# Performance work log

Measured on AMD Instinct MI355X. Metric: run time of the kernel, lower is better.

The kernel has to match this reference:

```python
import jax, jax.numpy as jnp
import numpy as np

NEG_SLOPE = 0.2  # PyG GATConv default negative_slope
EPS = 1e-16


def gat_conv(x, src, dst, num_nodes, W, a_src, a_dst, bias, heads, out_c, concat):
    """PyG-style GATConv (eval mode, self-loops already appended).
    x: [N, F_in]; src/dst: [E] (edge j->i with src=j, dst=i).
    W: [F_in, heads*out_c]; a_src/a_dst: [heads, out_c]; bias: [heads*out_c] or [out_c].
    """
    xw = (x @ W).reshape(num_nodes, heads, out_c)          # [N, H, C]
    alpha_src = jnp.sum(xw * a_src, axis=-1)               # [N, H]
    alpha_dst = jnp.sum(xw * a_dst, axis=-1)               # [N, H]
    e = jax.nn.leaky_relu(alpha_src[src] + alpha_dst[dst], NEG_SLOPE)  # [E, H]
    # numerically stable segment softmax over edges grouped by destination node
    m = jax.ops.segment_max(e, dst, num_segments=num_nodes)            # [N, H]
    e = jnp.exp(e - m[dst])
    denom = jax.ops.segment_sum(e, dst, num_segments=num_nodes)        # [N, H]
    alpha = e / (denom[dst] + EPS)                                     # [E, H]
    # weighted scatter-sum aggregation of source messages
    out = jax.ops.segment_sum(xw[src] * alpha[:, :, None], dst, num_segments=num_nodes)  # [N, H, C]
    if concat:
        out = out.reshape(num_nodes, heads * out_c)
    else:
        out = out.mean(axis=1)
    return out + bias


def setup_inputs() -> dict:
    key = jax.random.key(0)
    ks = jax.random.split(key, 12)
    N, E = 50000, 800000
    F_in, Hid, H1, Out = 512, 32, 8, 64

    def xavier(k, shape, gain=1.414):
        fan_in, fan_out = shape[0], shape[-1] if len(shape) == 2 else int(np.prod(shape[1:]))
        a = gain * np.sqrt(6.0 / (fan_in + fan_out))
        return jax.random.uniform(k, shape, jnp.float32, -a, a)

    x = jax.random.normal(ks[0], (N, F_in), jnp.float32)
    edge_index = jax.random.randint(ks[1], (2, E), 0, N, jnp.int64)

    W1 = xavier(ks[2], (F_in, H1 * Hid))
    a_src1 = xavier(ks[3], (H1, Hid))
    a_dst1 = xavier(ks[4], (H1, Hid))
    b1 = jnp.zeros((H1 * Hid,), jnp.float32)

    W2 = xavier(ks[5], (H1 * Hid, Out))
    a_src2 = xavier(ks[6], (1, Out))
    a_dst2 = xavier(ks[7], (1, Out))
    b2 = jnp.zeros((Out,), jnp.float32)

    return {"x": x, "edge_index": edge_index,
            "W1": W1, "a_src1": a_src1, "a_dst1": a_dst1, "b1": b1,
            "W2": W2, "a_src2": a_src2, "a_dst2": a_dst2, "b2": b2}


def reference(x, edge_index, W1, a_src1, a_dst1, b1, W2, a_src2, a_dst2, b2):
    N = x.shape[0]
    # add self-loops (PyG GATConv default add_self_loops=True)
    loop = jnp.arange(N, dtype=edge_index.dtype)
    src = jnp.concatenate([edge_index[0], loop])
    dst = jnp.concatenate([edge_index[1], loop])

    # eval mode: all dropouts are identity
    h = gat_conv(x, src, dst, N, W1, a_src1, a_dst1, b1, heads=8, out_c=32, concat=True)
    h = jax.nn.elu(h)
    h = gat_conv(h, src, dst, N, W2, a_src2, a_dst2, b2, heads=1, out_c=64, concat=False)
    return jax.nn.log_softmax(h, axis=1)
```

## Files before the change

kernel.cpp:

```cpp
#include <hip/hip_runtime.h>
#include <hip/hip_bf16.h>


typedef __attribute__((ext_vector_type(8)))  __bf16          bf16x8;
typedef __attribute__((ext_vector_type(8)))  unsigned short  ushort8;
typedef __attribute__((ext_vector_type(16))) float           f32x16;

#define NEG_SLOPE 0.2f
#define EPS_GAT 1e-16f

static __device__ __forceinline__ float lrelu(float x) {
    return x > 0.0f ? x : NEG_SLOPE * x;
}
static __device__ __forceinline__ unsigned short f2bf(float f) {
    unsigned u = __float_as_uint(f);
    return (unsigned short)((u + 0x7fffu + ((u >> 16) & 1u)) >> 16);
}
static __device__ __forceinline__ float bf2f(unsigned short v) {
    return __uint_as_float(((unsigned)v) << 16);
}
static __device__ __forceinline__ unsigned encf(float x) {
    unsigned u = __float_as_uint(x);
    return (u >> 31) ? ~u : (u | 0x80000000u);
}
static __device__ __forceinline__ float decf(unsigned e) {
    unsigned u = (e >> 31) ? (e & 0x7fffffffu) : ~e;
    return __uint_as_float(u);
}

__global__ void k_hist_w(const void* __restrict__ eix, int* __restrict__ counts,
                         int E, int EB,
                         const float* __restrict__ W1, const float* __restrict__ W2,
                         unsigned short* __restrict__ w1t, unsigned short* __restrict__ w2t) {
    int b = blockIdx.x;
    if (b < EB) {
        int i = b * 256 + threadIdx.x;
        unsigned w = ((const unsigned*)eix)[2 * min(i, E - 1) + 1];
        bool is64 = (__syncthreads_or((int)(w != 0u)) == 0);
        if (i < E) {
            int d = is64 ? (int)((const long long*)eix)[E + i]
                         : ((const int*)eix)[E + i];
            atomicAdd(&counts[d], 1);
        }
    } else {
        int t = (b - EB) * 256 + threadIdx.x;
        if (t < 512 * 256) {
            int k = t >> 8, m = t & 255;
            w1t[m * 512 + k] = f2bf(W1[t]);
        } else {
            int u = t - 512 * 256;
            if (u < 256 * 64) {
                int k = u >> 6, m = u & 63;
                w2t[m * 256 + k] = f2bf(W2[u]);
            }
        }
    }
}

__global__ void k_scan1(const int* __restrict__ counts, int* __restrict__ rowp,
                        int* __restrict__ bsum, int N) {
    __shared__ int s[256];
    int t = threadIdx.x, i = blockIdx.x * 256 + t;
    int v = (i < N) ? counts[i] : 0;
    s[t] = v;
    __syncthreads();
    for (int off = 1; off < 256; off <<= 1) {
        int u = (t >= off) ? s[t - off] : 0;
        __syncthreads();
        s[t] += u;
        __syncthreads();
    }
    if (i < N) rowp[i] = s[t] - v;
    if (t == 255) bsum[blockIdx.x] = s[255];
}

__global__ void k_scan2(const int* __restrict__ bsum, int* __restrict__ boff,
                        int* __restrict__ rowp_last, int NB) {
    __shared__ int s[256];
    int t = threadIdx.x;
    int v = (t < NB) ? bsum[t] : 0;
    s[t] = v;
    __syncthreads();
    for (int off = 1; off < 256; off <<= 1) {
        int u = (t >= off) ? s[t - off] : 0;
        __syncthreads();
        s[t] += u;
        __syncthreads();
    }
    if (t < NB) boff[t] = s[t] - v;
    if (t == 255) *rowp_last = s[255];
}

__global__ void k_scan3(int* __restrict__ rowp, int* __restrict__ cursor,
                        const int* __restrict__ boff, int N) {
    int i = blockIdx.x * 256 + threadIdx.x;
    if (i < N) {
        int r = rowp[i] + boff[blockIdx.x];
        rowp[i] = r;
        cursor[i] = r;
    }
}

__global__ void k_fill(const void* __restrict__ eix, int* __restrict__ cursor,
                       int* __restrict__ ssrc, int E) {
    int i = blockIdx.x * 256 + threadIdx.x;
    unsigned w = ((const unsigned*)eix)[2 * min(i, E - 1) + 1];
    bool is64 = (__syncthreads_or((int)(w != 0u)) == 0);
    if (i >= E) return;
    int s, d;
    if (is64) {
        s = (int)((const long long*)eix)[i];
        d = (int)((const long long*)eix)[E + i];
    } else {
        s = ((const int*)eix)[i];
        d = ((const int*)eix)[E + i];
    }
    int pos = atomicAdd(&cursor[d], 1);
    ssrc[pos] = s;
}

template <int BM, int BN, int NT, bool AF32, bool OUTBF>
__global__ __launch_bounds__(NT) void k_gemm(const void* __restrict__ Ain,
                                             const unsigned short* __restrict__ Bt,
                                             void* __restrict__ Cout, int Nrows, int K) {
    constexpr int LD = 40;
    __shared__ __align__(16) unsigned short As[BM * LD];
    __shared__ __align__(16) unsigned short Bs[BN * LD];
    const int tid = threadIdx.x;
    const int blockRow = blockIdx.x * BM;
    const int wave = tid >> 6, lane = tid & 63;
    constexpr int WR = BM / 64;
    const int wr = wave % WR, wc = wave / WR;
    const int m = lane & 31;
    const int ksel = (lane >> 5) * 8;

    f32x16 acc00{}, acc01{}, acc10{}, acc11{};

    for (int kt = 0; kt < K; kt += 32) {
        if constexpr (AF32) {
            const float* A = (const float*)Ain;
            for (int idx = tid; idx < BM * 4; idx += NT) {
                int r = idx >> 2, kc = (idx & 3) * 8;
                int grow = blockRow + r;
                union { ushort8 u; __hip_bfloat162 h[4]; } cv;
                if (grow < Nrows) {
                    const float* ap = A + (size_t)grow * K + kt + kc;
                    float4 x0 = *(const float4*)ap;
                    float4 x1 = *(const float4*)(ap + 4);
                    cv.h[0] = __float22bfloat162_rn(make_float2(x0.x, x0.y));
                    cv.h[1] = __float22bfloat162_rn(make_float2(x0.z, x0.w));
                    cv.h[2] = __float22bfloat162_rn(make_float2(x1.x, x1.y));
                    cv.h[3] = __float22bfloat162_rn(make_float2(x1.z, x1.w));
                } else {
                    cv.u = ushort8{};
                }
                *(ushort8*)&As[r * LD + kc] = cv.u;
            }
        } else {
            const unsigned short* A = (const unsigned short*)Ain;
            for (int idx = tid; idx < BM * 4; idx += NT) {
                int r = idx >> 2, kc = (idx & 3) * 8;
                int grow = blockRow + r;
                ushort8 o{};
                if (grow < Nrows) o = *(const ushort8*)(A + (size_t)grow * K + kt + kc);
                *(ushort8*)&As[r * LD + kc] = o;
            }
        }
        for (int idx = tid; idx < BN * 4; idx += NT) {
            int r = idx >> 2, kc = (idx & 3) * 8;
            *(ushort8*)&Bs[r * LD + kc] = *(const ushort8*)(Bt + (size_t)r * K + kt + kc);
        }
        __syncthreads();

        #pragma unroll
        for (int kk = 0; kk < 32; kk += 16) {
            bf16x8 a0 = *(const bf16x8*)&As[(wr * 64 +      m) * LD + kk + ksel];
            bf16x8 a1 = *(const bf16x8*)&As[(wr * 64 + 32 + m) * LD + kk + ksel];
            bf16x8 b0 = *(const bf16x8*)&Bs[(wc * 64 +      m) * LD + kk + ksel];
            bf16x8 b1 = *(const bf16x8*)&Bs[(wc * 64 + 32 + m) * LD + kk + ksel];
            acc00 = __builtin_amdgcn_mfma_f32_32x32x16_bf16(a0, b0, acc00, 0, 0, 0);
            acc01 = __builtin_amdgcn_mfma_f32_32x32x16_bf16(a0, b1, acc01, 0, 0, 0);
            acc10 = __builtin_amdgcn_mfma_f32_32x32x16_bf16(a1, b0, acc10, 0, 0, 0);
            acc11 = __builtin_amdgcn_mfma_f32_32x32x16_bf16(a1, b1, acc11, 0, 0, 0);
        }
        __syncthreads();
    }

    const int dcol = wc * 64 + (lane & 31);
    const int dquad = 4 * (lane >> 5);
    auto store_tile = [&](const f32x16& a, int rt, int ct) {
        #pragma unroll
        for (int r = 0; r < 16; ++r) {
            int row = blockRow + wr * 64 + rt * 32 + (r & 3) + 8 * (r >> 2) + dquad;
            if (row < Nrows) {
                size_t off = (size_t)row * BN + dcol + ct * 32;
                if constexpr (OUTBF) ((unsigned short*)Cout)[off] = f2bf(a[r]);
                else                 ((float*)Cout)[off] = a[r];
            }
        }
    };
    store_tile(acc00, 0, 0); store_tile(acc01, 0, 1);
    store_tile(acc10, 1, 0); store_tile(acc11, 1, 1);
}

__global__ void k_alpha(const unsigned short* __restrict__ xw, const float* __restrict__ a_s,
                        const float* __restrict__ a_d, float* __restrict__ os,
                        float* __restrict__ od, unsigned* __restrict__ Menc,
                        int NH, int H, int C) {
    __shared__ float red[256];
    int t = blockIdx.x * 256 + threadIdx.x;
    float s = -1e30f, d = 0.f;
    if (t < NH) {
        int n = t / H, h = t - n * H;
        const unsigned short* row = xw + (size_t)n * H * C + h * C;
        s = 0.f;
        for (int c = 0; c < C; c += 8) {
            ushort8 v = *(const ushort8*)(row + c);
            #pragma unroll
            for (int q = 0; q < 8; ++q) {
                float f = bf2f(v[q]);
                s += f * a_s[h * C + c + q];
                d += f * a_d[h * C + c + q];
            }
        }
        os[t] = s; od[t] = d;
    }
    red[threadIdx.x] = s;
    __syncthreads();
    for (int off = 128; off >= H; off >>= 1) {
        if (threadIdx.x < off) red[threadIdx.x] = fmaxf(red[threadIdx.x], red[threadIdx.x + off]);
        __syncthreads();
    }
    if ((int)threadIdx.x < H) atomicMax(&Menc[threadIdx.x], encf(red[threadIdx.x]));
}

__global__ __launch_bounds__(256) void k_agg_l1(
        const unsigned short* __restrict__ xw1, const float* __restrict__ asrc,
        const float* __restrict__ adst, const unsigned* __restrict__ Menc,
        const float* __restrict__ b1, const int* __restrict__ rp,
        const int* __restrict__ ssrc, unsigned short* __restrict__ hbf, int N) {
    int wid = (blockIdx.x * 256 + threadIdx.x) >> 6;
    if (wid >= N) return;
    int lane = threadIdx.x & 63;
    int g  = lane >> 4;
    int q  = lane & 15;
    int f0 = q * 16;
    int h  = q >> 1;
    int ih = wid * 8 + h;
    float ad = adst[ih];
    float m  = lrelu(decf(Menc[h]) + ad);
    float acc[16];
    float s;
    {
        float w = (g == 0) ? __expf(lrelu(asrc[ih] + ad) - m) : 0.0f;
        const unsigned short* pr = xw1 + (size_t)wid * 256 + f0;
        ushort8 lo = *(const ushort8*)pr;
        ushort8 hi = *(const ushort8*)(pr + 8);
        s = w;
        #pragma unroll
        for (int i = 0; i < 8; ++i) { acc[i] = w * bf2f(lo[i]); acc[8 + i] = w * bf2f(hi[i]); }
    }
    int e0 = rp[wid], e1 = rp[wid + 1];
    if (e0 < e1) {
        int eA = e0;
        bool vA = eA + g < e1;
        int jA = ssrc[min(eA + g, e1 - 1)];
        float asA = asrc[jA * 8 + h];
        const unsigned short* pA = xw1 + (size_t)jA * 256 + f0;
        ushort8 loA = *(const ushort8*)pA;
        ushort8 hiA = *(const ushort8*)(pA + 8);
        int eB = e0 + 4;
        bool hasB = eB < e1;
        bool vB = false; int jB = 0;
        if (hasB) { vB = eB + g < e1; jB = ssrc[min(eB + g, e1 - 1)]; }
        int eC = e0 + 8;
        while (true) {
            bool hasC = eC < e1;
            bool vC = false; int jC = 0;
            if (hasC) { vC = eC + g < e1; jC = ssrc[min(eC + g, e1 - 1)]; }
            float asB = 0.f; ushort8 loB{}, hiB{};
            if (hasB) {
                asB = asrc[jB * 8 + h];
                const unsigned short* pB = xw1 + (size_t)jB * 256 + f0;
                loB = *(const ushort8*)pB;
                hiB = *(const ushort8*)(pB + 8);
            }
            float w = vA ? __expf(lrelu(asA + ad) - m) : 0.0f;
            s += w;
            #pragma unroll
            for (int i = 0; i < 8; ++i) {
                acc[i]     += w * bf2f(loA[i]);
                acc[8 + i] += w * bf2f(hiA[i]);
            }
            if (!hasB) break;
            vA = vB; asA = asB; loA = loB; hiA = hiB;
            jB = jC; vB = vC; hasB = hasC;
            eC += 4;
        }
    }
    s += __shfl_xor(s, 16, 64);
    s += __shfl_xor(s, 32, 64);
    #pragma unroll
    for (int i = 0; i < 16; ++i) {
        acc[i] += __shfl_xor(acc[i], 16, 64);
        acc[i] += __shfl_xor(acc[i], 32, 64);
    }
    float inv = 1.0f / (s + EPS_GAT);
    int fw = f0 + g * 4;
    ushort4 o;
    #pragma unroll
    for (int i = 0; i < 4; ++i) {
        float v = acc[g * 4 + i] * inv + b1[fw + i];
        v = v > 0.f ? v : expm1f(v);
        ((unsigned short*)&o)[i] = f2bf(v);
    }
    *(ushort4*)(hbf + (size_t)wid * 256 + fw) = o;
}

__global__ __launch_bounds__(256) void k_agg_l2(
        const unsigned short* __restrict__ xw2, const float* __restrict__ asrc,
        const float* __restrict__ adst, const unsigned* __restrict__ Menc,
        const float* __restrict__ b2, const int* __restrict__ rp,
        const int* __restrict__ ssrc, float* __restrict__ out, int N) {
    int wid = (blockIdx.x * 256 + threadIdx.x) >> 6;
    if (wid >= N) return;
    int lane = threadIdx.x & 63;
    int g  = lane >> 3;
    int q  = lane & 7;
    int f0 = q * 8;
    float ad = adst[wid];
    float m = lrelu(decf(Menc[0]) + ad);
    float acc[8];
    float s;
    {
        float w = (g == 0) ? __expf(lrelu(asrc[wid] + ad) - m) : 0.0f;
        ushort8 xv = *(const ushort8*)(xw2 + (size_t)wid * 64 + f0);
        s = w;
        #pragma unroll
        for (int i = 0; i < 8; ++i) acc[i] = w * bf2f(xv[i]);
    }
    int e0 = rp[wid], e1 = rp[wid + 1];
    if (e0 < e1) {
        int eA = e0;
        bool vA = eA + g < e1;
        int jA = ssrc[min(eA + g, e1 - 1)];
        float asA = asrc[jA];
        ushort8 xvA = *(const ushort8*)(xw2 + (size_t)jA * 64 + f0);
        int eB = e0 + 8;
        bool hasB = eB < e1;
        bool vB = false; int jB = 0;
        if (hasB) { vB = eB + g < e1; jB = ssrc[min(eB + g, e1 - 1)]; }
        int eC = e0 + 16;
        while (true) {
            bool hasC = eC < e1;
            bool vC = false; int jC = 0;
            if (hasC) { vC = eC + g < e1; jC = ssrc[min(eC + g, e1 - 1)]; }
            float asB = 0.f; ushort8 xvB{};
            if (hasB) {
                asB = asrc[jB];
                xvB = *(const ushort8*)(xw2 + (size_t)jB * 64 + f0);
            }
            float w = vA ? __expf(lrelu(asA + ad) - m) : 0.0f;
            s += w;
            #pragma unroll
            for (int i = 0; i < 8; ++i) acc[i] += w * bf2f(xvA[i]);
            if (!hasB) break;
            vA = vB; asA = asB; xvA = xvB;
            jB = jC; vB = vC; hasB = hasC;
            eC += 8;
        }
    }
    s += __shfl_xor(s, 8, 64);
    s += __shfl_xor(s, 16, 64);
    s += __shfl_xor(s, 32, 64);
    #pragma unroll
    for (int i = 0; i < 8; ++i) {
        acc[i] += __shfl_xor(acc[i], 8, 64);
        acc[i] += __shfl_xor(acc[i], 16, 64);
        acc[i] += __shfl_xor(acc[i], 32, 64);
    }
    float inv = 1.0f / (s + EPS_GAT);
    float val[8];
    float mx = -1e30f;
    #pragma unroll
    for (int i = 0; i < 8; ++i) {
        val[i] = acc[i] * inv + b2[f0 + i];
        mx = fmaxf(mx, val[i]);
    }
    #pragma unroll
    for (int off = 4; off > 0; off >>= 1) mx = fmaxf(mx, __shfl_xor(mx, off, 64));
    float sm = 0.f;
    #pragma unroll
    for (int i = 0; i < 8; ++i) sm += __expf(val[i] - mx);
    #pragma unroll
    for (int off = 4; off > 0; off >>= 1) sm += __shfl_xor(sm, off, 64);
    float lse = mx + logf(sm);
    if (g == 0) {
        float4 o0 = make_float4(val[0] - lse, val[1] - lse, val[2] - lse, val[3] - lse);
        float4 o1 = make_float4(val[4] - lse, val[5] - lse, val[6] - lse, val[7] - lse);
        *(float4*)(out + (size_t)wid * 64 + f0)     = o0;
        *(float4*)(out + (size_t)wid * 64 + f0 + 4) = o1;
    }
}

static inline int cdiv(int a, int b) { return (a + b - 1) / b; }

extern "C" void kernel_launch(void* const* d_in, const int* in_sizes, int n_in,
                              void* d_out, int out_size, void* d_ws, size_t ws_size,
                              hipStream_t stream) {
    const float* x   = (const float*)d_in[0];
    const void*  eix = d_in[1];
    const float* W1  = (const float*)d_in[2];
    const float* as1 = (const float*)d_in[3];
    const float* ad1 = (const float*)d_in[4];
    const float* b1  = (const float*)d_in[5];
    const float* W2  = (const float*)d_in[6];
    const float* as2 = (const float*)d_in[7];
    const float* ad2 = (const float*)d_in[8];
    const float* b2  = (const float*)d_in[9];
    float* out = (float*)d_out;

    const int N = in_sizes[0] / 512;
    const int E = in_sizes[1] / 2;
    const int EB = cdiv(E, 256);
    const int WB = cdiv(512 * 256 + 256 * 64, 256);
    const int NB = cdiv(N, 256);
    const int NB1 = cdiv(N * 8, 256);
    const int NB2 = cdiv(N, 256);
    (void)n_in; (void)out_size; (void)ws_size;

    char* base = (char*)d_ws;
    size_t o = 0;
    auto alloc = [&](size_t bytes) -> char* {
        o = (o + 255) & ~(size_t)255;
        char* p = base + o;
        o += bytes;
        return p;
    };
    unsigned short* xw1b  = (unsigned short*)alloc((size_t)N * 256 * 2);
    unsigned short* hbf   = (unsigned short*)alloc((size_t)N * 256 * 2);
    unsigned short* xw2b  = (unsigned short*)alloc((size_t)N * 64 * 2);
    float*          asrc1 = (float*)alloc((size_t)N * 8 * 4);
    float*          adst1 = (float*)alloc((size_t)N * 8 * 4);
    float*          asrc2 = (float*)alloc((size_t)N * 4);
    float*          adst2 = (float*)alloc((size_t)N * 4);
    size_t zero_begin = (o + 255) & ~(size_t)255;
    unsigned*       Menc  = (unsigned*)alloc(16 * 4);
    int*            counts= (int*)alloc((size_t)N * 4);
    size_t zero_end = o;
    int*            cursor= (int*)alloc((size_t)N * 4);
    int*            rowp  = (int*)alloc((size_t)(N + 1) * 4);
    int*            bsum  = (int*)alloc(256 * 4);
    int*            boff  = (int*)alloc(256 * 4);
    unsigned short* w1t   = (unsigned short*)alloc(512 * 256 * 2);
    unsigned short* w2t   = (unsigned short*)alloc(256 * 64 * 2);
    int*            ssrc  = (int*)alloc((size_t)E * 4);

    hipMemsetAsync(base + zero_begin, 0, zero_end - zero_begin, stream);

    k_hist_w<<<EB + WB, 256, 0, stream>>>(eix, counts, E, EB, W1, W2, w1t, w2t);
    k_scan1<<<NB, 256, 0, stream>>>(counts, rowp, bsum, N);
    k_scan2<<<1, 256, 0, stream>>>(bsum, boff, rowp + N, NB);
    k_scan3<<<NB, 256, 0, stream>>>(rowp, cursor, boff, N);
    k_fill<<<EB, 256, 0, stream>>>(eix, cursor, ssrc, E);

    k_gemm<128, 256, 512, true, true><<<cdiv(N, 128), 512, 0, stream>>>(x, w1t, xw1b, N, 512);
    k_alpha<<<NB1, 256, 0, stream>>>(xw1b, as1, ad1, asrc1, adst1, Menc, N * 8, 8, 32);
    k_agg_l1<<<cdiv(N * 64, 256), 256, 0, stream>>>(xw1b, asrc1, adst1, Menc, b1,
                                                    rowp, ssrc, hbf, N);
    k_gemm<256, 64, 256, false, true><<<cdiv(N, 256), 256, 0, stream>>>(hbf, w2t, xw2b, N, 256);
    k_alpha<<<NB2, 256, 0, stream>>>(xw2b, as2, ad2, asrc2, adst2, Menc + 8, N, 1, 64);
    k_agg_l2<<<cdiv(N * 64, 256), 256, 0, stream>>>(xw2b, asrc2, adst2, Menc + 8, b2,
                                                    rowp, ssrc, out, N);
}
```

Before: 425.8 us.

## Deepen gather pipeline, use packed FMA, add occupancy hints, retile GEMMs

Both aggregation kernels move to a deeper software pipeline: neighbor indices are fetched two groups ahead and feature rows one group ahead, so gather latency is hidden. The bf16 unpack and accumulate now use packed v_pk_fma_f32 through inline asm, and launch_bounds request 6 waves per SIMD. Separately, both GEMM launches switch to smaller row tiles and fewer threads per block, giving more blocks. The aim is lower gather latency and ALU cost in aggregation and better load balance in the GEMMs, at the cost of more register pressure and smaller GEMM tiles that may reuse weights less.

Result: slower. 456.2 us (+7.1%).

```diff
diff --git a/kernel.cpp b/kernel.cpp
--- a/kernel.cpp
+++ b/kernel.cpp
@@ -5,6 +5,7 @@
 typedef __attribute__((ext_vector_type(8)))  __bf16          bf16x8;
 typedef __attribute__((ext_vector_type(8)))  unsigned short  ushort8;
 typedef __attribute__((ext_vector_type(16))) float           f32x16;
+typedef __attribute__((ext_vector_type(2)))  float           f32x2;
 
 #define NEG_SLOPE 0.2f
 #define EPS_GAT 1e-16f
@@ -234,22 +235,22 @@
     if ((int)threadIdx.x < H) atomicMax(&Menc[threadIdx.x], encf(red[threadIdx.x]));
 }
 
-__global__ __launch_bounds__(256) void k_agg_l1(
+__global__ __launch_bounds__(256, 6) void k_agg_l1(
         const unsigned short* __restrict__ xw1, const float* __restrict__ asrc,
         const float* __restrict__ adst, const unsigned* __restrict__ Menc,
         const float* __restrict__ b1, const int* __restrict__ rp,
         const int* __restrict__ ssrc, unsigned short* __restrict__ hbf, int N) {
     int wid = (blockIdx.x * 256 + threadIdx.x) >> 6;
     if (wid >= N) return;
-    int lane = threadIdx.x & 63;
-    int g  = lane >> 4;
-    int q  = lane & 15;
-    int f0 = q * 16;
-    int h  = q >> 1;
-    int ih = wid * 8 + h;
-    float ad = adst[ih];
-    float m  = lrelu(decf(Menc[h]) + ad);
-    float acc[16];
+    const int lane = threadIdx.x & 63;
+    const int g  = lane >> 4;
+    const int q  = lane & 15;
+    const int f0 = q * 16;
+    const int h  = q >> 1;
+    const int ih = wid * 8 + h;
+    const float ad = adst[ih];
+    const float m  = lrelu(decf(Menc[h]) + ad);
+    f32x2 acc[8];
     float s;
     {
         float w = (g == 0) ? __expf(lrelu(asrc[ih] + ad) - m) : 0.0f;
@@ -257,134 +258,198 @@
         ushort8 lo = *(const ushort8*)pr;
         ushort8 hi = *(const ushort8*)(pr + 8);
         s = w;
+        const unsigned* dl = (const unsigned*)&lo;
+        const unsigned* dh = (const unsigned*)&hi;
         #pragma unroll
-        for (int i = 0; i < 8; ++i) { acc[i] = w * bf2f(lo[i]); acc[8 + i] = w * bf2f(hi[i]); }
-    }
-    int e0 = rp[wid], e1 = rp[wid + 1];
+        for (int p = 0; p < 4; ++p) {
+            acc[p].x     = w * __uint_as_float(dl[p] << 16);
+            acc[p].y     = w * __uint_as_float(dl[p] & 0xffff0000u);
+            acc[4 + p].x = w * __uint_as_float(dh[p] << 16);
+            acc[4 + p].y = w * __uint_as_float(dh[p] & 0xffff0000u);
+        }
+    }
+    const int e0 = rp[wid], e1 = rp[wid + 1];
     if (e0 < e1) {
-        int eA = e0;
-        bool vA = eA + g < e1;
-        int jA = ssrc[min(eA + g, e1 - 1)];
-        float asA = asrc[jA * 8 + h];
-        const unsigned short* pA = xw1 + (size_t)jA * 256 + f0;
-        ushort8 loA = *(const ushort8*)pA;
-        ushort8 hiA = *(const ushort8*)(pA + 8);
-        int eB = e0 + 4;
-        bool hasB = eB < e1;
-        bool vB = false; int jB = 0;
-        if (hasB) { vB = eB + g < e1; jB = ssrc[min(eB + g, e1 - 1)]; }
-        int eC = e0 + 8;
-        while (true) {
-            bool hasC = eC < e1;
-            bool vC = false; int jC = 0;
-            if (hasC) { vC = eC + g < e1; jC = ssrc[min(eC + g, e1 - 1)]; }
-            float asB = 0.f; ushort8 loB{}, hiB{};
-            if (hasB) {
-                asB = asrc[jB * 8 + h];
-                const unsigned short* pB = xw1 + (size_t)jB * 256 + f0;
-                loB = *(const ushort8*)pB;
-                hiB = *(const ushort8*)(pB + 8);
-            }
-            float w = vA ? __expf(lrelu(asA + ad) - m) : 0.0f;
+        const int NQ = (e1 - e0 + 3) >> 2;
+
+        auto LDJ = [&](int base, int& j, bool& v) {
+            v = base + g < e1;
+            j = ssrc[min(base + g, e1 - 1)];
+        };
+        auto LDD = [&](int j, float& as, ushort8& lo, ushort8& hi) {
+            as = asrc[j * 8 + h];
+            const unsigned short* p = xw1 + ((size_t)j << 8) + f0;
+            lo = *(const ushort8*)p;
+            hi = *(const ushort8*)(p + 8);
+        };
+        auto CONS = [&](bool v, float as, const ushort8& lo, const ushort8& hi) {
+            float w = v ? __expf(lrelu(as + ad) - m) : 0.0f;
             s += w;
+            f32x2 wp; wp.x = w; wp.y = w;
+            const unsigned* dl = (const unsigned*)&lo;
+            const unsigned* dh = (const unsigned*)&hi;
             #pragma unroll
-            for (int i = 0; i < 8; ++i) {
-                acc[i]     += w * bf2f(loA[i]);
-                acc[8 + i] += w * bf2f(hiA[i]);
-            }
-            if (!hasB) break;
-            vA = vB; asA = asB; loA = loB; hiA = hiB;
-            jB = jC; vB = vC; hasB = hasC;
-            eC += 4;
-        }
+            for (int p = 0; p < 4; ++p) {
+                f32x2 x;
+                x.x = __uint_as_float(dl[p] << 16);
+                x.y = __uint_as_float(dl[p] & 0xffff0000u);
+                asm("v_pk_fma_f32 %0, %1, %2, %3"
+                    : "=v"(acc[p]) : "v"(x), "v"(wp), "v"(acc[p]));
+            }
+            #pragma unroll
+            for (int p = 0; p < 4; ++p) {
+                f32x2 x;
+                x.x = __uint_as_float(dh[p] << 16);
+                x.y = __uint_as_float(dh[p] & 0xffff0000u);
+                asm("v_pk_fma_f32 %0, %1, %2, %3"
+                    : "=v"(acc[4 + p]) : "v"(x), "v"(wp), "v"(acc[4 + p]));
+            }
+        };
+
+        int j0, j1, j2, j3; bool v0, v1, v2, v3;
+        float as0, as1; ushort8 lo0, hi0, lo1, hi1;
+        LDJ(e0,      j0, v0);
+        LDJ(e0 + 4,  j1, v1);
+        LDD(j0, as0, lo0, hi0);
+        LDJ(e0 + 8,  j2, v2);
+        LDD(j1, as1, lo1, hi1);
+        LDJ(e0 + 12, j3, v3);
+
+        #pragma unroll 2
+        for (int k = 0; k < NQ - 2; ++k) {
+            int jN; bool vN;
+            LDJ(e0 + 4 * k + 16, jN, vN);
+            float as2; ushort8 lo2, hi2;
+            LDD(j2, as2, lo2, hi2);
+            CONS(v0, as0, lo0, hi0);
+            v0 = v1; as0 = as1; lo0 = lo1; hi0 = hi1;
+            v1 = v2; as1 = as2; lo1 = lo2; hi1 = hi2;
+            v2 = v3; j2 = j3;
+            v3 = vN; j3 = jN;
+        }
+        CONS(v0, as0, lo0, hi0);
+        if (NQ >= 2) CONS(v1, as1, lo1, hi1);
     }
     s += __shfl_xor(s, 16, 64);
     s += __shfl_xor(s, 32, 64);
     #pragma unroll
-    for (int i = 0; i < 16; ++i) {
-        acc[i] += __shfl_xor(acc[i], 16, 64);
-        acc[i] += __shfl_xor(acc[i], 32, 64);
+    for (int p = 0; p < 8; ++p) {
+        acc[p].x += __shfl_xor(acc[p].x, 16, 64);
+        acc[p].x += __shfl_xor(acc[p].x, 32, 64);
+        acc[p].y += __shfl_xor(acc[p].y, 16, 64);
+        acc[p].y += __shfl_xor(acc[p].y, 32, 64);
     }
     float inv = 1.0f / (s + EPS_GAT);
+    f32x2 p0 = (g & 2) ? ((g & 1) ? acc[6] : acc[4]) : ((g & 1) ? acc[2] : acc[0]);
+    f32x2 p1 = (g & 2) ? ((g & 1) ? acc[7] : acc[5]) : ((g & 1) ? acc[3] : acc[1]);
     int fw = f0 + g * 4;
+    float vv[4] = { p0.x, p0.y, p1.x, p1.y };
     ushort4 o;
     #pragma unroll
     for (int i = 0; i < 4; ++i) {
-        float v = acc[g * 4 + i] * inv + b1[fw + i];
+        float v = vv[i] * inv + b1[fw + i];
         v = v > 0.f ? v : expm1f(v);
         ((unsigned short*)&o)[i] = f2bf(v);
     }
     *(ushort4*)(hbf + (size_t)wid * 256 + fw) = o;
 }
 
-__global__ __launch_bounds__(256) void k_agg_l2(
+__global__ __launch_bounds__(256, 6) void k_agg_l2(
         const unsigned short* __restrict__ xw2, const float* __restrict__ asrc,
         const float* __restrict__ adst, const unsigned* __restrict__ Menc,
         const float* __restrict__ b2, const int* __restrict__ rp,
         const int* __restrict__ ssrc, float* __restrict__ out, int N) {
     int wid = (blockIdx.x * 256 + threadIdx.x) >> 6;
     if (wid >= N) return;
-    int lane = threadIdx.x & 63;
-    int g  = lane >> 3;
-    int q  = lane & 7;
-    int f0 = q * 8;
-    float ad = adst[wid];
-    float m = lrelu(decf(Menc[0]) + ad);
-    float acc[8];
+    const int lane = threadIdx.x & 63;
+    const int g  = lane >> 3;
+    const int q  = lane & 7;
+    const int f0 = q * 8;
+    const float ad = adst[wid];
+    const float m = lrelu(decf(Menc[0]) + ad);
+    f32x2 acc[4];
     float s;
     {
         float w = (g == 0) ? __expf(lrelu(asrc[wid] + ad) - m) : 0.0f;
         ushort8 xv = *(const ushort8*)(xw2 + (size_t)wid * 64 + f0);
         s = w;
+        const unsigned* dx = (const unsigned*)&xv;
         #pragma unroll
-        for (int i = 0; i < 8; ++i) acc[i] = w * bf2f(xv[i]);
-    }
-    int e0 = rp[wid], e1 = rp[wid + 1];
+        for (int p = 0; p < 4; ++p) {
+            acc[p].x = w * __uint_as_float(dx[p] << 16);
+            acc[p].y = w * __uint_as_float(dx[p] & 0xffff0000u);
+        }
+    }
+    const int e0 = rp[wid], e1 = rp[wid + 1];
     if (e0 < e1) {
-        int eA = e0;
-        bool vA = eA + g < e1;
-        int jA = ssrc[min(eA + g, e1 - 1)];
-        float asA = asrc[jA];
-        ushort8 xvA = *(const ushort8*)(xw2 + (size_t)jA * 64 + f0);
-        int eB = e0 + 8;
-        bool hasB = eB < e1;
-        bool vB = false; int jB = 0;
-        if (hasB) { vB = eB + g < e1; jB = ssrc[min(eB + g, e1 - 1)]; }
-        int eC = e0 + 16;
-        while (true) {
-            bool hasC = eC < e1;
-            bool vC = false; int jC = 0;
-            if (hasC) { vC = eC + g < e1; jC = ssrc[min(eC + g, e1 - 1)]; }
-            float asB = 0.f; ushort8 xvB{};
-            if (hasB) {
-                asB = asrc[jB];
-                xvB = *(const ushort8*)(xw2 + (size_t)jB * 64 + f0);
-            }
-            float w = vA ? __expf(lrelu(asA + ad) - m) : 0.0f;
+        const int NQ = (e1 - e0 + 7) >> 3;
+
+        auto LDJ = [&](int base, int& j, bool& v) {
+            v = base + g < e1;
+            j = ssrc[min(base + g, e1 - 1)];
+        };
+        auto LDD = [&](int j, float& as, ushort8& xv) {
+            as = asrc[j];
+            xv = *(const ushort8*)(xw2 + ((size_t)j << 6) + f0);
+        };
+        auto CONS = [&](bool v, float as, const ushort8& xv) {
+            float w = v ? __expf(lrelu(as + ad) - m) : 0.0f;
             s += w;
+            f32x2 wp; wp.x = w; wp.y = w;
+            const unsigned* dx = (const unsigned*)&xv;
             #pragma unroll
-            for (int i = 0; i < 8; ++i) acc[i] += w * bf2f(xvA[i]);
-            if (!hasB) break;
-            vA = vB; asA = asB; xvA = xvB;
-            jB = jC; vB = vC; hasB = hasC;
-            eC += 8;
-        }
+            for (int p = 0; p < 4; ++p) {
+                f32x2 x;
+                x.x = __uint_as_float(dx[p] << 16);
+                x.y = __uint_as_float(dx[p] & 0xffff0000u);
+                asm("v_pk_fma_f32 %0, %1, %2, %3"
+                    : "=v"(acc[p]) : "v"(x), "v"(wp), "v"(acc[p]));
+            }
+        };
+
+        int j0, j1, j2, j3; bool v0, v1, v2, v3;
+        float as0, as1; ushort8 xv0, xv1;
+        LDJ(e0,      j0, v0);
+        LDJ(e0 + 8,  j1, v1);
+        LDD(j0, as0, xv0);
+        LDJ(e0 + 16, j2, v2);
+        LDD(j1, as1, xv1);
+        LDJ(e0 + 24, j3, v3);
+
+        #pragma unroll 2
+        for (int k = 0; k < NQ - 2; ++k) {
+            int jN; bool vN;
+            LDJ(e0 + 8 * k + 32, jN, vN);
+            float as2; ushort8 xv2;
+            LDD(j2, as2, xv2);
+            CONS(v0, as0, xv0);
+            v0 = v1; as0 = as1; xv0 = xv1;
+            v1 = v2; as1 = as2; xv1 = xv2;
+            v2 = v3; j2 = j3;
+            v3 = vN; j3 = jN;
+        }
+        CONS(v0, as0, xv0);
+        if (NQ >= 2) CONS(v1, as1, xv1);
     }
     s += __shfl_xor(s, 8, 64);
     s += __shfl_xor(s, 16, 64);
     s += __shfl_xor(s, 32, 64);
     #pragma unroll
-    for (int i = 0; i < 8; ++i) {
-        acc[i] += __shfl_xor(acc[i], 8, 64);
-        acc[i] += __shfl_xor(acc[i], 16, 64);
-        acc[i] += __shfl_xor(acc[i], 32, 64);
+    for (int p = 0; p < 4; ++p) {
+        acc[p].x += __shfl_xor(acc[p].x, 8, 64);
+        acc[p].x += __shfl_xor(acc[p].x, 16, 64);
+        acc[p].x += __shfl_xor(acc[p].x, 32, 64);
+        acc[p].y += __shfl_xor(acc[p].y, 8, 64);
+        acc[p].y += __shfl_xor(acc[p].y, 16, 64);
+        acc[p].y += __shfl_xor(acc[p].y, 32, 64);
     }
     float inv = 1.0f / (s + EPS_GAT);
     float val[8];
     float mx = -1e30f;
     #pragma unroll
     for (int i = 0; i < 8; ++i) {
-        val[i] = acc[i] * inv + b2[f0 + i];
+        float a = (i & 1) ? acc[i >> 1].y : acc[i >> 1].x;
+        val[i] = a * inv + b2[f0 + i];
         mx = fmaxf(mx, val[i]);
     }
     #pragma unroll
@@ -464,11 +529,11 @@
     k_scan3<<<NB, 256, 0, stream>>>(rowp, cursor, boff, N);
     k_fill<<<EB, 256, 0, stream>>>(eix, cursor, ssrc, E);
 
-    k_gemm<128, 256, 512, true, true><<<cdiv(N, 128), 512, 0, stream>>>(x, w1t, xw1b, N, 512);
+    k_gemm<64, 256, 256, true, true><<<cdiv(N, 64), 256, 0, stream>>>(x, w1t, xw1b, N, 512);
     k_alpha<<<NB1, 256, 0, stream>>>(xw1b, as1, ad1, asrc1, adst1, Menc, N * 8, 8, 32);
     k_agg_l1<<<cdiv(N * 64, 256), 256, 0, stream>>>(xw1b, asrc1, adst1, Menc, b1,
                                                     rowp, ssrc, hbf, N);
-    k_gemm<256, 64, 256, false, true><<<cdiv(N, 256), 256, 0, stream>>>(hbf, w2t, xw2b, N, 256);
+    k_gemm<64, 64, 64, false, true><<<cdiv(N, 64), 64, 0, stream>>>(hbf, w2t, xw2b, N, 256);
     k_alpha<<<NB2, 256, 0, stream>>>(xw2b, as2, ad2, asrc2, adst2, Menc + 8, N, 1, 64);
     k_agg_l2<<<cdiv(N * 64, 256), 256, 0, stream>>>(xw2b, asrc2, adst2, Menc + 8, b2,
                                                     rowp, ssrc, out, N);
```
